# Kernel optimization log

Hardware: AMD Instinct MI355X
Metric: run time of the kernel (lower is better)

Reference implementation:

```python
import jax, jax.numpy as jnp
import numpy as np

B, T, D = 8, 2048, 768
NUM_HEADS, KEY_DIM, VAL_DIM = 12, 64, 64
QKV_OUT = NUM_HEADS * (2 * KEY_DIM + VAL_DIM)  # 2304
MHK = NUM_HEADS * KEY_DIM  # 768


def setup_inputs() -> dict:
    key = jax.random.key(0)
    k = jax.random.split(key, 5)
    x = jax.random.normal(k[0], (B, T, D), dtype=jnp.float32)
    # Linear weights stored as [in, out] (equivalent to torch W.T)
    w_qkv = jax.random.normal(k[1], (D, QKV_OUT), dtype=jnp.float32) * (1.0 / np.sqrt(D))
    b_qkv = jax.random.normal(k[2], (QKV_OUT,), dtype=jnp.float32) * 0.02
    w_out = jax.random.normal(k[3], (NUM_HEADS * VAL_DIM, D), dtype=jnp.float32) * (1.0 / np.sqrt(NUM_HEADS * VAL_DIM))
    b_out = jax.random.normal(k[4], (D,), dtype=jnp.float32) * 0.02
    return {"x": x, "w_qkv": w_qkv, "b_qkv": b_qkv, "w_out": w_out, "b_out": b_out}


def reference(x, w_qkv, b_qkv, w_out, b_out):
    # qkv: [B, T, 2304]
    qkv = jnp.einsum('btd,de->bte', x, w_qkv) + b_qkv
    q = qkv[:, :, :MHK]            # [B, T, 768]
    k = qkv[:, :, MHK:2 * MHK]     # [B, T, 768]
    v = qkv[:, :, 2 * MHK:]        # [B, T, 768]
    # NOTE: faithful to source — contracts over the FULL num_heads*key_dim dim
    # (no head split), scale = sqrt(key_dim) only.
    scores = jnp.einsum('bqd,bkd->bqk', q, k) / jnp.sqrt(jnp.float32(KEY_DIM))
    attn = jax.nn.softmax(scores, axis=-1)        # [B, T, T]
    out = jnp.einsum('bqk,bkd->bqd', attn, v)      # [B, T, 768]
    return jnp.einsum('btd,de->bte', out, w_out) + b_out
```

## Files before the change

### kernel.cpp

```cpp
#include <hip/hip_runtime.h>

#define BB 8
#define TT 2048
#define DD 768
#define EE 2304
#define MM (BB * TT)
#define MHK_ 768
#define LOG2E 1.44269504088896340736f

typedef __attribute__((ext_vector_type(8))) _Float16 f16x8;
typedef __attribute__((ext_vector_type(4))) float f32x4;

typedef const __attribute__((address_space(1))) void* gp_t;
typedef __attribute__((address_space(3))) void* lp_t;

__device__ __forceinline__ float fast_exp2(float x) { return __builtin_amdgcn_exp2f(x); }

__global__ __launch_bounds__(256)
void k_prep(const float* __restrict__ x, const float* __restrict__ w_qkv,
            const float* __restrict__ w_out, _Float16* __restrict__ xh,
            _Float16* __restrict__ w_qkvT, _Float16* __restrict__ w_outT,
            float* __restrict__ lbuf) {
  __shared__ float tile[32][33];
  int bid = blockIdx.x;
  if (bid < 16) {
    lbuf[bid * 1024 + threadIdx.x * 4 + 0] = 0.f;
    lbuf[bid * 1024 + threadIdx.x * 4 + 1] = 0.f;
    lbuf[bid * 1024 + threadIdx.x * 4 + 2] = 0.f;
    lbuf[bid * 1024 + threadIdx.x * 4 + 3] = 0.f;
    return;
  }
  if (bid < 16 + 6144) {
    int idx = (bid - 16) * 256 + threadIdx.x;
    const float4* p = (const float4*)(x + idx * 8);
    float4 a = p[0], b = p[1];
    f16x8 o;
    o[0] = (_Float16)a.x; o[1] = (_Float16)a.y; o[2] = (_Float16)a.z; o[3] = (_Float16)a.w;
    o[4] = (_Float16)b.x; o[5] = (_Float16)b.y; o[6] = (_Float16)b.z; o[7] = (_Float16)b.w;
    *(f16x8*)(xh + idx * 8) = o;
    return;
  }
  const float* in;
  _Float16* out;
  int R, C, t;
  if (bid < 6160 + 1728) {
    t = bid - 6160; in = w_qkv; out = w_qkvT; R = DD; C = EE;
  } else {
    t = bid - 7888; in = w_out; out = w_outT; R = DD; C = DD;
  }
  const int tpr = C / 32;
  const int r0 = (t / tpr) * 32, c0 = (t - (t / tpr) * tpr) * 32;
  const int tx = threadIdx.x & 31, ty = threadIdx.x >> 5;
  for (int k = 0; k < 4; k++)
    tile[ty + k * 8][tx] = in[(size_t)(r0 + ty + k * 8) * C + c0 + tx];
  __syncthreads();
  for (int k = 0; k < 4; k++)
    out[(size_t)(c0 + ty + k * 8) * R + r0 + tx] = (_Float16)tile[tx][ty + k * 8];
}

__global__ __launch_bounds__(256)
void k_vt(const _Float16* __restrict__ qkv, _Float16* __restrict__ Vt) {
  __shared__ _Float16 tile[32][33];
  const int tx = threadIdx.x & 31;
  const int ty = threadIdx.x >> 5;
  const int t0 = blockIdx.x * 32;
  const int d0 = blockIdx.y * 32;
  const int b = blockIdx.z;
  for (int r = 0; r < 4; r++) {
    int t = t0 + ty + r * 8;
    tile[ty + r * 8][tx] = qkv[(size_t)(b * TT + t) * EE + 2 * MHK_ + d0 + tx];
  }
  __syncthreads();
  for (int r = 0; r < 4; r++) {
    int d = d0 + ty + r * 8;
    Vt[((size_t)b * DD + d) * TT + t0 + tx] = tile[tx][ty + r * 8];
  }
}

template<bool OUT_F16, bool HAS_BIAS, bool QSCALE, bool EXP_LSUM, bool ROWSCALE>
__global__ __launch_bounds__(256)
void k_gemm(const _Float16* __restrict__ A, const _Float16* __restrict__ Bt,
            const float* __restrict__ bias, void* __restrict__ Cv,
            float* __restrict__ lbuf,
            int lda, int ldb, int ldc, int Kd,
            long long strideA, long long strideB, long long strideC,
            int gx, int gyp, float qscale) {
  __shared__ __align__(16) _Float16 As[2][128 * 32];
  __shared__ __align__(16) _Float16 Bs[2][128 * 32];
  const int tid = threadIdx.x;
  const int lane = tid & 63;
  const int w = tid >> 6;
  const int quad = lane >> 4;
  const int l16 = lane & 15;

  const int bid = blockIdx.x;
  const int xcd = bid & 7;
  int local = bid >> 3;
  const int perz = gx * gyp;
  const int z = local / perz;
  local -= z * perz;
  const int lm = local / gx;
  const int nblk = local - lm * gx;
  const int m0 = (xcd * gyp + lm) * 128;
  const int n0 = nblk * 128;

  const int wr = (w >> 1) * 64;
  const int wc = (w & 1) * 64;

  const int srow = tid >> 2;
  const int scc = ((tid & 3) ^ ((tid >> 2) & 3)) * 8;
  const _Float16* Abase = A + (long long)z * strideA + (size_t)(m0 + srow) * lda + scc;
  const _Float16* Bbase = Bt + (long long)z * strideB + (size_t)(n0 + srow) * ldb + scc;
  const size_t a64 = (size_t)64 * lda;
  const size_t b64 = (size_t)64 * ldb;
  const int wbase = (w * 16) * 32;

  f32x4 acc[4][4];
  for (int i = 0; i < 4; i++)
    for (int j = 0; j < 4; j++)
      for (int r = 0; r < 4; r++) acc[i][j][r] = 0.f;

  const int fsw = (quad ^ (l16 & 3)) * 8;

  __builtin_amdgcn_global_load_lds((gp_t)(Abase), (lp_t)(&As[0][wbase]), 16, 0, 0);
  __builtin_amdgcn_global_load_lds((gp_t)(Abase + a64), (lp_t)(&As[0][wbase + 64 * 32]), 16, 0, 0);
  __builtin_amdgcn_global_load_lds((gp_t)(Bbase), (lp_t)(&Bs[0][wbase]), 16, 0, 0);
  __builtin_amdgcn_global_load_lds((gp_t)(Bbase + b64), (lp_t)(&Bs[0][wbase + 64 * 32]), 16, 0, 0);

  const int niter = Kd >> 5;
  for (int it = 0; it < niter; it++) {
    const int p = it & 1;
    __syncthreads();
    if (it + 1 < niter) {
      const int pn = p ^ 1;
      const size_t ko = (size_t)(it + 1) * 32;
      __builtin_amdgcn_global_load_lds((gp_t)(Abase + ko), (lp_t)(&As[pn][wbase]), 16, 0, 0);
      __builtin_amdgcn_global_load_lds((gp_t)(Abase + ko + a64), (lp_t)(&As[pn][wbase + 64 * 32]), 16, 0, 0);
      __builtin_amdgcn_global_load_lds((gp_t)(Bbase + ko), (lp_t)(&Bs[pn][wbase]), 16, 0, 0);
      __builtin_amdgcn_global_load_lds((gp_t)(Bbase + ko + b64), (lp_t)(&Bs[pn][wbase + 64 * 32]), 16, 0, 0);
    }
    f16x8 af[4], bf[4];
    for (int i = 0; i < 4; i++) af[i] = *(const f16x8*)&As[p][(wr + i * 16 + l16) * 32 + fsw];
    for (int j = 0; j < 4; j++) bf[j] = *(const f16x8*)&Bs[p][(wc + j * 16 + l16) * 32 + fsw];
    for (int i = 0; i < 4; i++)
      for (int j = 0; j < 4; j++)
        acc[i][j] = __builtin_amdgcn_mfma_f32_16x16x32_f16(af[i], bf[j], acc[i][j], 0, 0, 0);
  }

  const long long cbase = (long long)z * strideC;

  if (EXP_LSUM) {
    float psum[4][4];
    for (int i = 0; i < 4; i++)
      for (int r = 0; r < 4; r++) psum[i][r] = 0.f;
    for (int j = 0; j < 4; j++) {
      int col = n0 + wc + j * 16 + l16;
      for (int i = 0; i < 4; i++) {
        int row = m0 + wr + i * 16 + quad * 4;
        for (int r = 0; r < 4; r++) {
          float p = fast_exp2(acc[i][j][r] - 24.f);
          psum[i][r] += p;
          ((_Float16*)Cv)[cbase + (size_t)(row + r) * ldc + col] = (_Float16)p;
        }
      }
    }
    for (int i = 0; i < 4; i++)
      for (int r = 0; r < 4; r++) {
        float v = psum[i][r];
        v += __shfl_xor(v, 1, 64);
        v += __shfl_xor(v, 2, 64);
        v += __shfl_xor(v, 4, 64);
        v += __shfl_xor(v, 8, 64);
        if (l16 == 0)
          atomicAdd(&lbuf[z * TT + m0 + wr + i * 16 + quad * 4 + r], v);
      }
    return;
  }

  float invr[4][4];
  if (ROWSCALE) {
    for (int i = 0; i < 4; i++)
      for (int r = 0; r < 4; r++)
        invr[i][r] = 1.f / lbuf[z * TT + m0 + wr + i * 16 + quad * 4 + r];
  }

  for (int j = 0; j < 4; j++) {
    int col = n0 + wc + j * 16 + l16;
    float bv = HAS_BIAS ? bias[col] : 0.f;
    float sc = 1.f;
    if (QSCALE && col < MHK_) sc = qscale;
    for (int i = 0; i < 4; i++) {
      int row = m0 + wr + i * 16 + quad * 4;
      for (int r = 0; r < 4; r++) {
        float v = (acc[i][j][r] + bv) * sc;
        if (ROWSCALE) v = acc[i][j][r] * invr[i][r];
        if (OUT_F16)
          ((_Float16*)Cv)[cbase + (size_t)(row + r) * ldc + col] = (_Float16)v;
        else
          ((float*)Cv)[cbase + (size_t)(row + r) * ldc + col] = v;
      }
    }
  }
}

extern "C" void kernel_launch(void* const* d_in, const int* in_sizes, int n_in,
                              void* d_out, int out_size, void* d_ws, size_t ws_size,
                              hipStream_t stream) {
  const float* x = (const float*)d_in[0];
  const float* w_qkv = (const float*)d_in[1];
  const float* b_qkv = (const float*)d_in[2];
  const float* w_out = (const float*)d_in[3];
  const float* b_out = (const float*)d_in[4];

  _Float16* ws = (_Float16*)d_ws;
  _Float16* w_qkvT = ws;
  _Float16* w_outT = w_qkvT + (size_t)EE * DD;
  _Float16* qkv = w_outT + (size_t)DD * DD;
  _Float16* Vt = qkv + (size_t)MM * EE;
  _Float16* P = Vt + (size_t)BB * DD * TT;
  _Float16* ctx = P + (size_t)BB * TT * TT;
  float* lbuf = (float*)(ctx + (size_t)MM * DD);
  _Float16* xh = ctx + (size_t)MM * DD + MM * 2;

  k_prep<<<8464, 256, 0, stream>>>(x, w_qkv, w_out, xh, w_qkvT, w_outT, lbuf);
  k_gemm<true, true, true, false, false><<<2304, 256, 0, stream>>>(
      xh, w_qkvT, b_qkv, qkv, nullptr, DD, DD, EE, DD, 0, 0, 0, 18, 16, 0.125f * LOG2E);
  k_vt<<<dim3(TT / 32, DD / 32, BB), 256, 0, stream>>>(qkv, Vt);
  k_gemm<true, false, false, true, false><<<2048, 256, 0, stream>>>(
      qkv, qkv + MHK_, nullptr, P, lbuf, EE, EE, TT, DD,
      (long long)TT * EE, (long long)TT * EE, (long long)TT * TT, 16, 2, 1.f);
  k_gemm<true, false, false, false, true><<<768, 256, 0, stream>>>(
      P, Vt, nullptr, ctx, lbuf, TT, TT, DD, TT,
      (long long)TT * TT, (long long)DD * TT, (long long)TT * DD, 6, 2, 1.f);
  k_gemm<false, true, false, false, false><<<768, 256, 0, stream>>>(
      ctx, w_outT, b_out, d_out, nullptr, DD, DD, DD, DD, 0, 0, 0, 6, 16, 1.f);
}
```

Measured before the change: 405.9 us.

## Reassociate out-projection into V before attention and drop V transpose

Result: no change. 411.7 us (+1.4%).

```diff
diff --git a/kernel.cpp b/kernel.cpp
--- a/kernel.cpp
+++ b/kernel.cpp
@@ -58,26 +58,7 @@
     out[(size_t)(c0 + ty + k * 8) * R + r0 + tx] = (_Float16)tile[tx][ty + k * 8];
 }
 
-__global__ __launch_bounds__(256)
-void k_vt(const _Float16* __restrict__ qkv, _Float16* __restrict__ Vt) {
-  __shared__ _Float16 tile[32][33];
-  const int tx = threadIdx.x & 31;
-  const int ty = threadIdx.x >> 5;
-  const int t0 = blockIdx.x * 32;
-  const int d0 = blockIdx.y * 32;
-  const int b = blockIdx.z;
-  for (int r = 0; r < 4; r++) {
-    int t = t0 + ty + r * 8;
-    tile[ty + r * 8][tx] = qkv[(size_t)(b * TT + t) * EE + 2 * MHK_ + d0 + tx];
-  }
-  __syncthreads();
-  for (int r = 0; r < 4; r++) {
-    int d = d0 + ty + r * 8;
-    Vt[((size_t)b * DD + d) * TT + t0 + tx] = tile[tx][ty + r * 8];
-  }
-}
-
-template<bool OUT_F16, bool HAS_BIAS, bool QSCALE, bool EXP_LSUM, bool ROWSCALE>
+template<int NJ, bool OUT_F16, bool HAS_BIAS, bool QSCALE, bool EXP_LSUM, bool ROWSCALE, bool XN>
 __global__ __launch_bounds__(256)
 void k_gemm(const _Float16* __restrict__ A, const _Float16* __restrict__ Bt,
             const float* __restrict__ bias, void* __restrict__ Cv,
@@ -85,8 +66,9 @@
             int lda, int ldb, int ldc, int Kd,
             long long strideA, long long strideB, long long strideC,
             int gx, int gyp, float qscale) {
+  const int TN = NJ * 32;
   __shared__ __align__(16) _Float16 As[2][128 * 32];
-  __shared__ __align__(16) _Float16 Bs[2][128 * 32];
+  __shared__ __align__(16) _Float16 Bs[2][NJ * 32 * 32];
   const int tid = threadIdx.x;
   const int lane = tid & 63;
   const int w = tid >> 6;
@@ -99,13 +81,13 @@
   const int perz = gx * gyp;
   const int z = local / perz;
   local -= z * perz;
-  const int lm = local / gx;
-  const int nblk = local - lm * gx;
-  const int m0 = (xcd * gyp + lm) * 128;
-  const int n0 = nblk * 128;
+  const int i1 = local / gx;
+  const int i0 = local - i1 * gx;
+  const int m0 = XN ? i0 * 128 : (xcd * gyp + i1) * 128;
+  const int n0 = XN ? (xcd * gyp + i1) * TN : i0 * TN;
 
   const int wr = (w >> 1) * 64;
-  const int wc = (w & 1) * 64;
+  const int wc = (w & 1) * (TN / 2);
 
   const int srow = tid >> 2;
   const int scc = ((tid & 3) ^ ((tid >> 2) & 3)) * 8;
@@ -115,9 +97,9 @@
   const size_t b64 = (size_t)64 * ldb;
   const int wbase = (w * 16) * 32;
 
-  f32x4 acc[4][4];
+  f32x4 acc[4][NJ];
   for (int i = 0; i < 4; i++)
-    for (int j = 0; j < 4; j++)
+    for (int j = 0; j < NJ; j++)
       for (int r = 0; r < 4; r++) acc[i][j][r] = 0.f;
 
   const int fsw = (quad ^ (l16 & 3)) * 8;
@@ -125,7 +107,8 @@
   __builtin_amdgcn_global_load_lds((gp_t)(Abase), (lp_t)(&As[0][wbase]), 16, 0, 0);
   __builtin_amdgcn_global_load_lds((gp_t)(Abase + a64), (lp_t)(&As[0][wbase + 64 * 32]), 16, 0, 0);
   __builtin_amdgcn_global_load_lds((gp_t)(Bbase), (lp_t)(&Bs[0][wbase]), 16, 0, 0);
-  __builtin_amdgcn_global_load_lds((gp_t)(Bbase + b64), (lp_t)(&Bs[0][wbase + 64 * 32]), 16, 0, 0);
+  if (NJ == 4)
+    __builtin_amdgcn_global_load_lds((gp_t)(Bbase + b64), (lp_t)(&Bs[0][wbase + 64 * 32]), 16, 0, 0);
 
   const int niter = Kd >> 5;
   for (int it = 0; it < niter; it++) {
@@ -137,13 +120,14 @@
       __builtin_amdgcn_global_load_lds((gp_t)(Abase + ko), (lp_t)(&As[pn][wbase]), 16, 0, 0);
       __builtin_amdgcn_global_load_lds((gp_t)(Abase + ko + a64), (lp_t)(&As[pn][wbase + 64 * 32]), 16, 0, 0);
       __builtin_amdgcn_global_load_lds((gp_t)(Bbase + ko), (lp_t)(&Bs[pn][wbase]), 16, 0, 0);
-      __builtin_amdgcn_global_load_lds((gp_t)(Bbase + ko + b64), (lp_t)(&Bs[pn][wbase + 64 * 32]), 16, 0, 0);
+      if (NJ == 4)
+        __builtin_amdgcn_global_load_lds((gp_t)(Bbase + ko + b64), (lp_t)(&Bs[pn][wbase + 64 * 32]), 16, 0, 0);
     }
-    f16x8 af[4], bf[4];
+    f16x8 af[4], bf[NJ];
     for (int i = 0; i < 4; i++) af[i] = *(const f16x8*)&As[p][(wr + i * 16 + l16) * 32 + fsw];
-    for (int j = 0; j < 4; j++) bf[j] = *(const f16x8*)&Bs[p][(wc + j * 16 + l16) * 32 + fsw];
-    for (int i = 0; i < 4; i++)
-      for (int j = 0; j < 4; j++)
+    for (int j = 0; j < NJ; j++) bf[j] = *(const f16x8*)&Bs[p][(wc + j * 16 + l16) * 32 + fsw];
+    for (int i = 0; i < 4; i++)
+      for (int j = 0; j < NJ; j++)
         acc[i][j] = __builtin_amdgcn_mfma_f32_16x16x32_f16(af[i], bf[j], acc[i][j], 0, 0, 0);
   }
 
@@ -153,7 +137,7 @@
     float psum[4][4];
     for (int i = 0; i < 4; i++)
       for (int r = 0; r < 4; r++) psum[i][r] = 0.f;
-    for (int j = 0; j < 4; j++) {
+    for (int j = 0; j < NJ; j++) {
       int col = n0 + wc + j * 16 + l16;
       for (int i = 0; i < 4; i++) {
         int row = m0 + wr + i * 16 + quad * 4;
@@ -184,16 +168,21 @@
         invr[i][r] = 1.f / lbuf[z * TT + m0 + wr + i * 16 + quad * 4 + r];
   }
 
-  for (int j = 0; j < 4; j++) {
+  for (int j = 0; j < NJ; j++) {
     int col = n0 + wc + j * 16 + l16;
     float bv = HAS_BIAS ? bias[col] : 0.f;
-    float sc = 1.f;
-    if (QSCALE && col < MHK_) sc = qscale;
     for (int i = 0; i < 4; i++) {
       int row = m0 + wr + i * 16 + quad * 4;
       for (int r = 0; r < 4; r++) {
-        float v = (acc[i][j][r] + bv) * sc;
-        if (ROWSCALE) v = acc[i][j][r] * invr[i][r];
+        float v = acc[i][j][r];
+        if (QSCALE) {
+          v += bv;
+          if (col < MHK_) v *= qscale;
+        } else if (ROWSCALE) {
+          v = v * invr[i][r] + bv;
+        } else {
+          v += bv;
+        }
         if (OUT_F16)
           ((_Float16*)Cv)[cbase + (size_t)(row + r) * ldc + col] = (_Float16)v;
         else
@@ -216,22 +205,21 @@
   _Float16* w_qkvT = ws;
   _Float16* w_outT = w_qkvT + (size_t)EE * DD;
   _Float16* qkv = w_outT + (size_t)DD * DD;
-  _Float16* Vt = qkv + (size_t)MM * EE;
-  _Float16* P = Vt + (size_t)BB * DD * TT;
-  _Float16* ctx = P + (size_t)BB * TT * TT;
-  float* lbuf = (float*)(ctx + (size_t)MM * DD);
-  _Float16* xh = ctx + (size_t)MM * DD + MM * 2;
+  _Float16* VWt = qkv + (size_t)MM * EE;
+  _Float16* P = VWt + (size_t)BB * DD * TT;
+  float* lbuf = (float*)(P + (size_t)BB * TT * TT);
+  _Float16* xh = (_Float16*)(lbuf + MM);
 
   k_prep<<<8464, 256, 0, stream>>>(x, w_qkv, w_out, xh, w_qkvT, w_outT, lbuf);
-  k_gemm<true, true, true, false, false><<<2304, 256, 0, stream>>>(
+  k_gemm<4, true, true, true, false, false, false><<<2304, 256, 0, stream>>>(
       xh, w_qkvT, b_qkv, qkv, nullptr, DD, DD, EE, DD, 0, 0, 0, 18, 16, 0.125f * LOG2E);
-  k_vt<<<dim3(TT / 32, DD / 32, BB), 256, 0, stream>>>(qkv, Vt);
-  k_gemm<true, false, false, true, false><<<2048, 256, 0, stream>>>(
+  k_gemm<2, true, false, false, false, false, true><<<1536, 256, 0, stream>>>(
+      w_outT, qkv + 2 * MHK_, nullptr, VWt, nullptr, DD, EE, TT, DD,
+      0, (long long)TT * EE, (long long)DD * TT, 6, 4, 1.f);
+  k_gemm<4, true, false, false, true, false, false><<<2048, 256, 0, stream>>>(
       qkv, qkv + MHK_, nullptr, P, lbuf, EE, EE, TT, DD,
       (long long)TT * EE, (long long)TT * EE, (long long)TT * TT, 16, 2, 1.f);
-  k_gemm<true, false, false, false, true><<<768, 256, 0, stream>>>(
-      P, Vt, nullptr, ctx, lbuf, TT, TT, DD, TT,
-      (long long)TT * TT, (long long)DD * TT, (long long)TT * DD, 6, 2, 1.f);
-  k_gemm<false, true, false, false, false><<<768, 256, 0, stream>>>(
-      ctx, w_outT, b_out, d_out, nullptr, DD, DD, DD, DD, 0, 0, 0, 6, 16, 1.f);
+  k_gemm<2, false, true, false, false, true, false><<<1536, 256, 0, stream>>>(
+      P, VWt, b_out, d_out, lbuf, TT, TT, DD, TT,
+      (long long)TT * TT, (long long)DD * TT, (long long)TT * DD, 12, 2, 1.f);
 }
```
